# Kernel tuning notes

Measured on AMD Instinct MI355X. Metric: run time of the kernel, lower is better.

Reference implementation:

```python
import jax, jax.numpy as jnp
import numpy as np

B, S, D, H = 2, 2048, 1024, 16
DK = D // H


def setup_inputs() -> dict:
    key = jax.random.key(0)
    ks = jax.random.split(key, 12)
    sc = 0.02
    inp = {
        "q": jax.random.normal(ks[0], (B, S, D), jnp.float32),
        "k": jax.random.normal(ks[1], (B, S, D), jnp.float32),
        "v": jax.random.normal(ks[2], (B, S, D), jnp.float32),
        "mask": jnp.ones((B, S, S), jnp.int32),
        "Wq": jax.random.normal(ks[3], (D, D), jnp.float32) * sc,
        "bq": jnp.zeros((D,), jnp.float32),
        "Wk": jax.random.normal(ks[4], (D, D), jnp.float32) * sc,
        "bk": jnp.zeros((D,), jnp.float32),
        "Wv": jax.random.normal(ks[5], (D, D), jnp.float32) * sc,
        "bv": jnp.zeros((D,), jnp.float32),
        "Wo": jax.random.normal(ks[6], (D, D), jnp.float32) * sc,
        "bo": jnp.zeros((D,), jnp.float32),
    }
    return inp


def _split_heads(x):
    # [B,S,D] -> [B,H,S,DK]
    b, s, _ = x.shape
    return x.reshape(b, s, H, DK).transpose(0, 2, 1, 3)


def reference(q, k, v, mask, Wq, bq, Wk, bk, Wv, bv, Wo, bo):
    qh = _split_heads(q @ Wq.T + bq)
    kh = _split_heads(k @ Wk.T + bk)
    vh = _split_heads(v @ Wv.T + bv)
    scale = 1.0 / jnp.sqrt(jnp.float32(DK))
    scores = jnp.einsum("bhqd,bhkd->bhqk", qh, kh) * scale  # [B,H,S,S]
    scores = jnp.where(mask[:, None, :, :] == 0, jnp.float32(-1e9), scores)
    probs = jax.nn.softmax(scores, axis=-1)  # dropout p=0.0 -> identity
    out = jnp.einsum("bhqk,bhkd->bhqd", probs, vh)  # [B,H,S,DK]
    concat = out.transpose(0, 2, 1, 3).reshape(q.shape[0], -1, D)
    return concat @ Wo.T + bo
```

## Files before the change

### kernel.cpp

```cpp
#include <hip/hip_runtime.h>
#include <stdint.h>

#define Bsz 2
#define Ssz 2048
#define Dsz 1024
#define Hsz 16
#define DKsz 64

typedef __attribute__((ext_vector_type(8))) short sh8;
typedef __attribute__((ext_vector_type(4))) float fx4;
typedef __attribute__((ext_vector_type(16))) float fx16;
typedef __attribute__((ext_vector_type(4))) unsigned ux4;

__device__ __forceinline__ unsigned short f2bf(float x) {
  uint32_t u = __builtin_bit_cast(uint32_t, x);
  uint32_t r = (u + 0x7fffu + ((u >> 16) & 1u)) >> 16;
  return (unsigned short)r;
}

__device__ __forceinline__ fx4 mfma16(sh8 a, sh8 b, fx4 c) {
  return __builtin_amdgcn_mfma_f32_16x16x32_bf16(a, b, c, 0, 0, 0);
}

__device__ __forceinline__ fx16 mfma32(sh8 a, sh8 b, fx16 c) {
  return __builtin_amdgcn_mfma_f32_32x32x16_bf16(a, b, c, 0, 0, 0);
}

__device__ __forceinline__ void g2l16(const void* g, void* l) {
  __builtin_amdgcn_global_load_lds((const __attribute__((address_space(1))) void*)g,
                                   (__attribute__((address_space(3))) void*)l, 16, 0, 0);
}

__device__ __forceinline__ float fexp2(float x) {
#if __has_builtin(__builtin_amdgcn_exp2f)
  return __builtin_amdgcn_exp2f(x);
#else
  return exp2f(x);
#endif
}

__device__ __forceinline__ unsigned cvtpk(float lo, float hi) {
  unsigned r;
  asm("v_cvt_pk_bf16_f32 %0, %1, %2" : "=v"(r) : "v"(lo), "v"(hi));
  return r;
}

__device__ __forceinline__ void plswap(unsigned& a, unsigned& b) {
  asm("v_permlane32_swap_b32 %0, %1" : "+v"(a), "+v"(b));
}

__device__ __forceinline__ void build_pa(const fx16& p, sh8& pa0, sh8& pa1) {
  unsigned w0 = cvtpk(p[0], p[1]), w1 = cvtpk(p[2], p[3]);
  unsigned w2 = cvtpk(p[4], p[5]), w3 = cvtpk(p[6], p[7]);
  unsigned w4 = cvtpk(p[8], p[9]), w5 = cvtpk(p[10], p[11]);
  unsigned w6 = cvtpk(p[12], p[13]), w7 = cvtpk(p[14], p[15]);
  plswap(w0, w2);
  plswap(w1, w3);
  ux4 u0 = {w0, w1, w2, w3};
  pa0 = __builtin_bit_cast(sh8, u0);
  plswap(w4, w6);
  plswap(w5, w7);
  ux4 u1 = {w4, w5, w6, w7};
  pa1 = __builtin_bit_cast(sh8, u1);
}

__global__ __launch_bounds__(256) void convert_kernel(
    const float* __restrict__ wq, const float* __restrict__ wk, const float* __restrict__ wv,
    const float* __restrict__ wo, const int* __restrict__ mask,
    unsigned short* __restrict__ wqb, unsigned short* __restrict__ wkb,
    unsigned short* __restrict__ wvb, unsigned short* __restrict__ wob,
    int* __restrict__ flag) {
  const int NW = Dsz * Dsz / 4;
  const int NC = 4 * NW;
  const int NM = Bsz * Ssz * Ssz / 4;
  const int total = NC + NM;
  int bad = 0;
  for (int i = blockIdx.x * blockDim.x + threadIdx.x; i < total; i += gridDim.x * blockDim.x) {
    if (i >= NC) {
      int4 m = ((const int4*)mask)[i - NC];
      if (m.x == 0 || m.y == 0 || m.z == 0 || m.w == 0) bad = 1;
      continue;
    }
    int t = i / NW, off = i - t * NW;
    const float* src = (t == 0) ? wq : ((t == 1) ? wk : ((t == 2) ? wv : wo));
    unsigned short* dst = (t == 0) ? wqb : ((t == 1) ? wkb : ((t == 2) ? wvb : wob));
    float4 x = ((const float4*)src)[off];
    ushort4 o;
    o.x = f2bf(x.x); o.y = f2bf(x.y); o.z = f2bf(x.z); o.w = f2bf(x.w);
    ((ushort4*)dst)[off] = o;
  }
  if (bad) atomicAnd(flag, 0);
}

__global__ void flag_init_kernel(int* flag) {
  if (threadIdx.x == 0 && blockIdx.x == 0) flag[0] = 1;
}

__global__ __launch_bounds__(256) void proj_qkv_kernel(
    const float* __restrict__ qf, const float* __restrict__ kf, const float* __restrict__ vf,
    const unsigned short* __restrict__ wqb, const unsigned short* __restrict__ wkb,
    const unsigned short* __restrict__ wvb,
    const float* __restrict__ bq, const float* __restrict__ bk, const float* __restrict__ bv,
    unsigned short* __restrict__ qh, unsigned short* __restrict__ kh,
    unsigned short* __restrict__ vt) {
  __shared__ __align__(16) unsigned short SMEM[17408];
  unsigned short* As0 = SMEM;
  unsigned short* As1 = SMEM + 4096;
  unsigned short* Bs0 = SMEM + 8192;
  unsigned short* Bs1 = SMEM + 12288;
  unsigned short* Ts = SMEM;
  const int z = blockIdx.z;
  const float* X = (z == 0) ? qf : ((z == 1) ? kf : vf);
  const unsigned short* W = (z == 0) ? wqb : ((z == 1) ? wkb : wvb);
  const float* bias = (z == 0) ? bq : ((z == 1) ? bk : bv);
  const int m0 = blockIdx.x * 128, n0 = blockIdx.y * 128;
  const int tid = threadIdx.x, lane = tid & 63, wid = tid >> 6;
  const int wm = wid >> 1, wn = wid & 1;
  const int c = lane & 15, g = lane >> 4;
  fx4 acc[4][4] = {};

  auto LOADA = [&](int k0, float4* a) {
#pragma unroll
    for (int i = 0; i < 4; i++) {
      int c4 = i * 256 + tid;
      a[i] = *(const float4*)(X + (size_t)(m0 + (c4 >> 3)) * Dsz + k0 + (c4 & 7) * 4);
    }
  };
  auto WRITEA = [&](const float4* a, unsigned short* As) {
#pragma unroll
    for (int i = 0; i < 4; i++) {
      int c4 = i * 256 + tid;
      uint2 w;
      w.x = cvtpk(a[i].x, a[i].y);
      w.y = cvtpk(a[i].z, a[i].w);
      *(uint2*)&As[(c4 >> 3) * 32 + (c4 & 7) * 4] = w;
    }
  };
  auto G2LB = [&](int k0, unsigned short* Bs) {
#pragma unroll
    for (int i = 0; i < 2; i++) {
      int e = i * 256 + tid;
      g2l16(W + (size_t)(n0 + (e >> 2)) * Dsz + k0 + (e & 3) * 8,
            (char*)Bs + (size_t)(i * 256 + wid * 64) * 16);
    }
  };
  auto COMPUTE = [&](const unsigned short* As, const unsigned short* Bs) {
    sh8 af[4], bfr[4];
#pragma unroll
    for (int m = 0; m < 4; m++)
      af[m] = *(const sh8*)&As[(wm * 64 + m * 16 + c) * 32 + g * 8];
#pragma unroll
    for (int n = 0; n < 4; n++)
      bfr[n] = *(const sh8*)&Bs[(wn * 64 + n * 16 + c) * 32 + g * 8];
#pragma unroll
    for (int m = 0; m < 4; m++)
#pragma unroll
      for (int n = 0; n < 4; n++)
        acc[m][n] = mfma16(af[m], bfr[n], acc[m][n]);
  };

  float4 aA[4], aB[4];
  LOADA(0, aA);
  G2LB(0, Bs0);
  WRITEA(aA, As0);
  __syncthreads();
#pragma unroll 1
  for (int j = 0; j < 16; j++) {
    const int k0 = j * 64;
    if (k0 + 32 < Dsz) { LOADA(k0 + 32, aB); G2LB(k0 + 32, Bs1); }
    COMPUTE(As0, Bs0);
    if (k0 + 32 < Dsz) WRITEA(aB, As1);
    __syncthreads();
    if (k0 + 64 < Dsz) { LOADA(k0 + 64, aA); G2LB(k0 + 64, Bs0); }
    if (k0 + 32 < Dsz) COMPUTE(As1, Bs1);
    if (k0 + 64 < Dsz) WRITEA(aA, As0);
    __syncthreads();
  }

  const float CE = 0.18033688011112042f;
  if (z < 2) {
    unsigned short* O = (z == 0) ? qh : kh;
    const float sc = (z == 0) ? CE : 1.0f;
#pragma unroll
    for (int n = 0; n < 4; n++) {
      int j = n0 + wn * 64 + n * 16 + c;
      float bj = bias[j];
      int h = j >> 6, dk = j & 63;
#pragma unroll
      for (int m = 0; m < 4; m++)
#pragma unroll
        for (int r = 0; r < 4; r++) {
          int i = m0 + wm * 64 + m * 16 + g * 4 + r;
          int b = i >> 11, s = i & 2047;
          O[(((size_t)(b * Hsz + h) * Ssz + s) << 6) + dk] = f2bf((acc[m][n][r] + bj) * sc);
        }
    }
  } else {
#pragma unroll
    for (int n = 0; n < 4; n++) {
      int nl = wn * 64 + n * 16 + c;
      float bj = bias[n0 + nl];
#pragma unroll
      for (int m = 0; m < 4; m++)
#pragma unroll
        for (int r = 0; r < 4; r++) {
          int ml = wm * 64 + m * 16 + g * 4 + r;
          Ts[nl * 136 + ml] = f2bf(acc[m][n][r] + bj);
        }
    }
    __syncthreads();
    int b = m0 >> 11, sbase = m0 & 2047;
#pragma unroll
    for (int it = 0; it < 8; it++) {
      int ch = it * 256 + tid;
      int row = ch >> 4, off = ch & 15;
      sh8 dv = *(const sh8*)&Ts[row * 136 + off * 8];
      int j = n0 + row;
      int h = j >> 6, dk = j & 63;
      *(sh8*)&vt[(size_t)((b * Hsz + h) * DKsz + dk) * Ssz + sbase + off * 8] = dv;
    }
  }
}

__global__ __launch_bounds__(512, 4) void attn_kernel(
    const unsigned short* __restrict__ qh, const unsigned short* __restrict__ kh,
    const unsigned short* __restrict__ vt, const int* __restrict__ mask,
    const int* __restrict__ flag, unsigned short* __restrict__ concat) {
  __shared__ __align__(16) unsigned short SM[2][2][2][4096];
  const int tid = threadIdx.x, lane = tid & 63, wid = tid >> 6;
  const int grp = wid >> 2, w4 = wid & 3;
  const int fid = blockIdx.y * gridDim.x + blockIdx.x;
  const int logical = (fid & 7) * 64 + (fid >> 3);
  const int bh = logical >> 4, qblk = logical & 15;
  const int b = bh >> 4, h = bh & 15;
  const int q0 = qblk * 128 + w4 * 32;
  const int c = lane & 31, hi = lane >> 5;
  const int cs = c & 7;
  const int kvbase = grp * (Ssz / 2);
  const unsigned short* Qb = qh + ((size_t)bh * Ssz + q0) * DKsz;
  const unsigned short* Kb = kh + (size_t)bh * Ssz * DKsz;
  const unsigned short* Vb = vt + (size_t)bh * DKsz * Ssz;
  const int ch0 = w4 * 128 + lane;
  const int ch1 = ch0 + 64;
  const int r0 = ch0 >> 3, sl0 = (ch0 & 7) ^ (r0 & 7);
  const int r1 = ch1 >> 3, sl1 = (ch1 & 7) ^ (r1 & 7);
  const int koff0 = r0 * DKsz + sl0 * 8, koff1 = r1 * DKsz + sl1 * 8;
  const size_t voff0 = (size_t)r0 * Ssz + sl0 * 8, voff1 = (size_t)r1 * Ssz + sl1 * 8;

  sh8 qf[4];
#pragma unroll
  for (int ks = 0; ks < 4; ks++)
    qf[ks] = *(const sh8*)&Qb[(size_t)c * DKsz + ks * 16 + hi * 8];
  const bool allones = (flag[0] != 0);
  float lsum = 0.f;
  fx16 o0 = {}, o1 = {};

  auto STAGE = [&](int bufi, int kv0) {
    const unsigned short* ksrc = Kb + (size_t)kv0 * DKsz;
    char* kdst = (char*)&SM[0][grp][bufi][0] + w4 * 2048;
    g2l16(ksrc + koff0, kdst);
    g2l16(ksrc + koff1, kdst + 1024);
    const unsigned short* vsrc = Vb + kv0;
    char* vdst = (char*)&SM[1][grp][bufi][0] + w4 * 2048;
    g2l16(vsrc + voff0, vdst);
    g2l16(vsrc + voff1, vdst + 1024);
  };

  const int NT = (Ssz / 2) / 64;
  STAGE(0, kvbase);
  asm volatile("s_waitcnt vmcnt(0)" ::: "memory");
  __builtin_amdgcn_s_barrier();
  asm volatile("" ::: "memory");

  for (int t = 0; t < NT; ++t) {
    const int cur = t & 1;
    const int kv0 = kvbase + t * 64;
    if (t + 1 < NT) STAGE(cur ^ 1, kv0 + 64);
    const unsigned short* Kt = &SM[0][grp][cur][0];
    const unsigned short* Vt = &SM[1][grp][cur][0];
    fx16 s0 = {}, s1 = {};
    __builtin_amdgcn_s_setprio(1);
#pragma unroll
    for (int ks = 0; ks < 4; ks++) {
      int sl = (2 * ks + hi) ^ cs;
      sh8 ka = *(const sh8*)&Kt[(c * 8 + sl) * 8];
      sh8 kb2 = *(const sh8*)&Kt[((32 + c) * 8 + sl) * 8];
      s0 = mfma32(ka, qf[ks], s0);
      s1 = mfma32(kb2, qf[ks], s1);
    }
    __builtin_amdgcn_s_setprio(0);
    if (!allones) {
      const int* mrow = mask + ((size_t)b * Ssz + (q0 + c)) * Ssz + kv0;
#pragma unroll
      for (int r = 0; r < 16; r++) {
        int kv = (r & 3) + 8 * (r >> 2) + 4 * hi;
        if (mrow[kv] == 0) s0[r] = -1e9f;
        if (mrow[32 + kv] == 0) s1[r] = -1e9f;
      }
    }
    fx16 p0v, p1v;
#pragma unroll
    for (int r = 0; r < 16; r++) {
      p0v[r] = fexp2(s0[r]);
      p1v[r] = fexp2(s1[r]);
    }
    sh8 pa[4];
    build_pa(p0v, pa[0], pa[1]);
    build_pa(p1v, pa[2], pa[3]);
    __builtin_amdgcn_s_setprio(1);
#pragma unroll
    for (int ks = 0; ks < 4; ks++) {
      int sl = (2 * ks + hi) ^ cs;
      sh8 v0f = *(const sh8*)&Vt[(c * 8 + sl) * 8];
      sh8 v1f = *(const sh8*)&Vt[((32 + c) * 8 + sl) * 8];
      o0 = mfma32(v0f, pa[ks], o0);
      o1 = mfma32(v1f, pa[ks], o1);
    }
    __builtin_amdgcn_s_setprio(0);
    float sm[16];
#pragma unroll
    for (int r = 0; r < 16; r++) sm[r] = p0v[r] + p1v[r];
#pragma unroll
    for (int w = 8; w >= 1; w >>= 1)
#pragma unroll
      for (int r = 0; r < w; r++) sm[r] += sm[r + w];
    lsum += sm[0];
    asm volatile("s_waitcnt vmcnt(0)" ::: "memory");
    __builtin_amdgcn_s_barrier();
    asm volatile("" ::: "memory");
  }

  float* CB = (float*)&SM[0][0][0][0];
  float* CBl = CB + 4 * 32 * 68;
  if (grp == 1) {
#pragma unroll
    for (int k4 = 0; k4 < 4; k4++) {
      fx4 a = {o0[4 * k4], o0[4 * k4 + 1], o0[4 * k4 + 2], o0[4 * k4 + 3]};
      *(fx4*)&CB[(w4 * 32 + c) * 68 + 8 * k4 + 4 * hi] = a;
      fx4 bvv = {o1[4 * k4], o1[4 * k4 + 1], o1[4 * k4 + 2], o1[4 * k4 + 3]};
      *(fx4*)&CB[(w4 * 32 + c) * 68 + 32 + 8 * k4 + 4 * hi] = bvv;
    }
    CBl[w4 * 64 + hi * 32 + c] = lsum;
  }
  __syncthreads();
  if (grp == 0) {
#pragma unroll
    for (int k4 = 0; k4 < 4; k4++) {
      fx4 a = *(const fx4*)&CB[(w4 * 32 + c) * 68 + 8 * k4 + 4 * hi];
      o0[4 * k4] += a[0]; o0[4 * k4 + 1] += a[1]; o0[4 * k4 + 2] += a[2]; o0[4 * k4 + 3] += a[3];
      fx4 bvv = *(const fx4*)&CB[(w4 * 32 + c) * 68 + 32 + 8 * k4 + 4 * hi];
      o1[4 * k4] += bvv[0]; o1[4 * k4 + 1] += bvv[1]; o1[4 * k4 + 2] += bvv[2]; o1[4 * k4 + 3] += bvv[3];
    }
    lsum += CBl[w4 * 64 + hi * 32 + c];
    lsum += __shfl_xor(lsum, 32);
    float linv = 1.0f / lsum;
    unsigned short* Ob = concat + ((size_t)b * Ssz + q0 + c) * Dsz + h * DKsz;
#pragma unroll
    for (int rg = 0; rg < 4; rg++) {
      ushort4 w;
      w.x = f2bf(o0[rg * 4 + 0] * linv);
      w.y = f2bf(o0[rg * 4 + 1] * linv);
      w.z = f2bf(o0[rg * 4 + 2] * linv);
      w.w = f2bf(o0[rg * 4 + 3] * linv);
      *(ushort4*)&Ob[8 * rg + 4 * hi] = w;
      ushort4 w2;
      w2.x = f2bf(o1[rg * 4 + 0] * linv);
      w2.y = f2bf(o1[rg * 4 + 1] * linv);
      w2.z = f2bf(o1[rg * 4 + 2] * linv);
      w2.w = f2bf(o1[rg * 4 + 3] * linv);
      *(ushort4*)&Ob[32 + 8 * rg + 4 * hi] = w2;
    }
  }
}

__global__ __launch_bounds__(256) void outproj_kernel(
    const unsigned short* __restrict__ Xc, const unsigned short* __restrict__ wob,
    const float* __restrict__ bo, float* __restrict__ out) {
  __shared__ __align__(16) unsigned short As[128 * 32];
  __shared__ __align__(16) unsigned short Bs[128 * 32];
  const int m0 = blockIdx.x * 128, n0 = blockIdx.y * 128;
  const int tid = threadIdx.x, lane = tid & 63, wid = tid >> 6;
  const int wm = wid >> 1, wn = wid & 1;
  const int c = lane & 15, g = lane >> 4;
  fx4 acc[4][4] = {};
  for (int k0 = 0; k0 < Dsz; k0 += 32) {
#pragma unroll
    for (int i = 0; i < 2; i++) {
      int e = i * 256 + tid;
      g2l16(Xc + (size_t)(m0 + (e >> 2)) * Dsz + k0 + (e & 3) * 8,
            (char*)As + (size_t)(i * 256 + wid * 64) * 16);
      g2l16(wob + (size_t)(n0 + (e >> 2)) * Dsz + k0 + (e & 3) * 8,
            (char*)Bs + (size_t)(i * 256 + wid * 64) * 16);
    }
    __syncthreads();
    sh8 af[4], bfr[4];
#pragma unroll
    for (int m = 0; m < 4; m++)
      af[m] = *(const sh8*)&As[(wm * 64 + m * 16 + c) * 32 + g * 8];
#pragma unroll
    for (int n = 0; n < 4; n++)
      bfr[n] = *(const sh8*)&Bs[(wn * 64 + n * 16 + c) * 32 + g * 8];
#pragma unroll
    for (int m = 0; m < 4; m++)
#pragma unroll
      for (int n = 0; n < 4; n++)
        acc[m][n] = mfma16(af[m], bfr[n], acc[m][n]);
    __syncthreads();
  }
#pragma unroll
  for (int n = 0; n < 4; n++) {
    int j = n0 + wn * 64 + n * 16 + c;
    float bj = bo[j];
#pragma unroll
    for (int m = 0; m < 4; m++)
#pragma unroll
      for (int r = 0; r < 4; r++) {
        int i = m0 + wm * 64 + m * 16 + g * 4 + r;
        out[(size_t)i * Dsz + j] = acc[m][n][r] + bj;
      }
  }
}

extern "C" void kernel_launch(void* const* d_in, const int* in_sizes, int n_in,
                              void* d_out, int out_size, void* d_ws, size_t ws_size,
                              hipStream_t stream) {
  const float* q = (const float*)d_in[0];
  const float* k = (const float*)d_in[1];
  const float* v = (const float*)d_in[2];
  const int* mask = (const int*)d_in[3];
  const float* Wq = (const float*)d_in[4];
  const float* bq = (const float*)d_in[5];
  const float* Wk = (const float*)d_in[6];
  const float* bk = (const float*)d_in[7];
  const float* Wv = (const float*)d_in[8];
  const float* bv = (const float*)d_in[9];
  const float* Wo = (const float*)d_in[10];
  const float* bo = (const float*)d_in[11];
  float* out = (float*)d_out;
  char* ws = (char*)d_ws;
  const size_t MB = 1 << 20;
  unsigned short* wqb = (unsigned short*)(ws + 0 * MB);
  unsigned short* wkb = (unsigned short*)(ws + 2 * MB);
  unsigned short* wvb = (unsigned short*)(ws + 4 * MB);
  unsigned short* wob = (unsigned short*)(ws + 6 * MB);
  unsigned short* qhp = (unsigned short*)(ws + 8 * MB);
  unsigned short* khp = (unsigned short*)(ws + 16 * MB);
  unsigned short* vtp = (unsigned short*)(ws + 24 * MB);
  unsigned short* cc  = (unsigned short*)(ws + 32 * MB);
  int* flag = (int*)(ws + 40 * MB);

  hipLaunchKernelGGL(flag_init_kernel, dim3(1), dim3(64), 0, stream, flag);
  hipLaunchKernelGGL(convert_kernel, dim3(1024), dim3(256), 0, stream,
                     Wq, Wk, Wv, Wo, mask, wqb, wkb, wvb, wob, flag);
  hipLaunchKernelGGL(proj_qkv_kernel, dim3(32, 8, 3), dim3(256), 0, stream,
                     q, k, v, wqb, wkb, wvb, bq, bk, bv, qhp, khp, vtp);
  hipLaunchKernelGGL(attn_kernel, dim3(16, 32), dim3(512), 0, stream,
                     qhp, khp, vtp, mask, flag, cc);
  hipLaunchKernelGGL(outproj_kernel, dim3(32, 8), dim3(256), 0, stream,
                     cc, wob, bo, out);
}
```

Before: 139.1 us.

## Deepen QKV projection prefetch pipeline and stage Q/K epilogue stores through LDS

The QKV projection main loop becomes a single-step pipeline. A-operand register loads are issued two k-steps ahead, and partial vmcnt waits with raw s_barrier replace full __syncthreads, so global latency overlaps with MFMA work. The Q/K epilogue now writes bf16 results into shared memory first and then emits 16-byte vectorized global stores, replacing scattered 2-byte stores. This adds LDS traffic and an extra barrier, and it depends on the hand-counted vmcnt values being correct.

```diff
diff --git a/kernel.cpp b/kernel.cpp
--- a/kernel.cpp
+++ b/kernel.cpp
@@ -104,10 +104,6 @@
     unsigned short* __restrict__ qh, unsigned short* __restrict__ kh,
     unsigned short* __restrict__ vt) {
   __shared__ __align__(16) unsigned short SMEM[17408];
-  unsigned short* As0 = SMEM;
-  unsigned short* As1 = SMEM + 4096;
-  unsigned short* Bs0 = SMEM + 8192;
-  unsigned short* Bs1 = SMEM + 12288;
   unsigned short* Ts = SMEM;
   const int z = blockIdx.z;
   const float* X = (z == 0) ? qf : ((z == 1) ? kf : vf);
@@ -118,40 +114,49 @@
   const int wm = wid >> 1, wn = wid & 1;
   const int c = lane & 15, g = lane >> 4;
   fx4 acc[4][4] = {};
-
-  auto LOADA = [&](int k0, float4* a) {
+  const int NSTEP = Dsz / 32;
+
+  float4 rA[2][4];
+
+  auto LOADA = [&](int t, float4* r) {
+    const int k0 = t * 32;
 #pragma unroll
     for (int i = 0; i < 4; i++) {
       int c4 = i * 256 + tid;
-      a[i] = *(const float4*)(X + (size_t)(m0 + (c4 >> 3)) * Dsz + k0 + (c4 & 7) * 4);
+      r[i] = *(const float4*)(X + (size_t)(m0 + (c4 >> 3)) * Dsz + k0 + (c4 & 7) * 4);
     }
   };
-  auto WRITEA = [&](const float4* a, unsigned short* As) {
+  auto WRITEA = [&](const float4* r, int buf) {
+    unsigned short* dst = SMEM + buf * 4096;
 #pragma unroll
     for (int i = 0; i < 4; i++) {
       int c4 = i * 256 + tid;
       uint2 w;
-      w.x = cvtpk(a[i].x, a[i].y);
-      w.y = cvtpk(a[i].z, a[i].w);
-      *(uint2*)&As[(c4 >> 3) * 32 + (c4 & 7) * 4] = w;
+      w.x = cvtpk(r[i].x, r[i].y);
+      w.y = cvtpk(r[i].z, r[i].w);
+      *(uint2*)&dst[(c4 >> 3) * 32 + (c4 & 7) * 4] = w;
     }
   };
-  auto G2LB = [&](int k0, unsigned short* Bs) {
+  auto G2LB = [&](int t, int buf) {
+    const int k0 = t * 32;
+    unsigned short* dst = SMEM + 8192 + buf * 4096;
 #pragma unroll
     for (int i = 0; i < 2; i++) {
       int e = i * 256 + tid;
       g2l16(W + (size_t)(n0 + (e >> 2)) * Dsz + k0 + (e & 3) * 8,
-            (char*)Bs + (size_t)(i * 256 + wid * 64) * 16);
+            (char*)dst + (size_t)(i * 256 + wid * 64) * 16);
     }
   };
-  auto COMPUTE = [&](const unsigned short* As, const unsigned short* Bs) {
+  auto COMPUTE = [&](int buf) {
+    const unsigned short* A_ = SMEM + buf * 4096;
+    const unsigned short* B_ = SMEM + 8192 + buf * 4096;
     sh8 af[4], bfr[4];
 #pragma unroll
     for (int m = 0; m < 4; m++)
-      af[m] = *(const sh8*)&As[(wm * 64 + m * 16 + c) * 32 + g * 8];
+      af[m] = *(const sh8*)&A_[(wm * 64 + m * 16 + c) * 32 + g * 8];
 #pragma unroll
     for (int n = 0; n < 4; n++)
-      bfr[n] = *(const sh8*)&Bs[(wn * 64 + n * 16 + c) * 32 + g * 8];
+      bfr[n] = *(const sh8*)&B_[(wn * 64 + n * 16 + c) * 32 + g * 8];
 #pragma unroll
     for (int m = 0; m < 4; m++)
 #pragma unroll
@@ -159,23 +164,31 @@
         acc[m][n] = mfma16(af[m], bfr[n], acc[m][n]);
   };
 
-  float4 aA[4], aB[4];
-  LOADA(0, aA);
-  G2LB(0, Bs0);
-  WRITEA(aA, As0);
+  LOADA(0, rA[0]);
+  G2LB(0, 0);
+  LOADA(1, rA[1]);
+  WRITEA(rA[0], 0);
+  asm volatile("s_waitcnt vmcnt(4)" ::: "memory");
+  __builtin_amdgcn_s_barrier();
+  asm volatile("" ::: "memory");
+
+#pragma unroll 1
+  for (int t = 0; t < NSTEP; ++t) {
+    const int cur = t & 1;
+    if (t + 1 < NSTEP) G2LB(t + 1, cur ^ 1);
+    if (t + 2 < NSTEP) LOADA(t + 2, rA[t & 1]);
+    COMPUTE(cur);
+    if (t + 1 < NSTEP) {
+      WRITEA(rA[(t + 1) & 1], cur ^ 1);
+      if (t + 2 < NSTEP)
+        asm volatile("s_waitcnt vmcnt(4)" ::: "memory");
+      else
+        asm volatile("s_waitcnt vmcnt(0)" ::: "memory");
+      __builtin_amdgcn_s_barrier();
+      asm volatile("" ::: "memory");
+    }
+  }
   __syncthreads();
-#pragma unroll 1
-  for (int j = 0; j < 16; j++) {
-    const int k0 = j * 64;
-    if (k0 + 32 < Dsz) { LOADA(k0 + 32, aB); G2LB(k0 + 32, Bs1); }
-    COMPUTE(As0, Bs0);
-    if (k0 + 32 < Dsz) WRITEA(aB, As1);
-    __syncthreads();
-    if (k0 + 64 < Dsz) { LOADA(k0 + 64, aA); G2LB(k0 + 64, Bs0); }
-    if (k0 + 32 < Dsz) COMPUTE(As1, Bs1);
-    if (k0 + 64 < Dsz) WRITEA(aA, As0);
-    __syncthreads();
-  }
 
   const float CE = 0.18033688011112042f;
   if (z < 2) {
@@ -183,17 +196,27 @@
     const float sc = (z == 0) ? CE : 1.0f;
 #pragma unroll
     for (int n = 0; n < 4; n++) {
-      int j = n0 + wn * 64 + n * 16 + c;
-      float bj = bias[j];
+      int nl = wn * 64 + n * 16 + c;
+      float bj = bias[n0 + nl];
+#pragma unroll
+      for (int m = 0; m < 4; m++)
+#pragma unroll
+        for (int r = 0; r < 4; r++) {
+          int ml = wm * 64 + m * 16 + g * 4 + r;
+          Ts[ml * 136 + nl] = f2bf((acc[m][n][r] + bj) * sc);
+        }
+    }
+    __syncthreads();
+#pragma unroll
+    for (int it = 0; it < 8; it++) {
+      int ch = it * 256 + tid;
+      int row = ch >> 4, off = ch & 15;
+      sh8 dv = *(const sh8*)&Ts[row * 136 + off * 8];
+      int i = m0 + row;
+      int b = i >> 11, s = i & 2047;
+      int j = n0 + off * 8;
       int h = j >> 6, dk = j & 63;
-#pragma unroll
-      for (int m = 0; m < 4; m++)
-#pragma unroll
-        for (int r = 0; r < 4; r++) {
-          int i = m0 + wm * 64 + m * 16 + g * 4 + r;
-          int b = i >> 11, s = i & 2047;
-          O[(((size_t)(b * Hsz + h) * Ssz + s) << 6) + dk] = f2bf((acc[m][n][r] + bj) * sc);
-        }
+      *(sh8*)&O[(((size_t)(b * Hsz + h) * Ssz + s) << 6) + dk] = dv;
     }
   } else {
 #pragma unroll
```

Measured after the change: 215.9 us. 1.55x slower.

## Load fp32 A tiles directly to LDS with swizzle, stage Q/K epilogue stores

Applied to the files above, without the earlier changes.

The QKV projection now copies fp32 activation tiles straight into LDS through async global-to-LDS copies with an XOR swizzle, converting to bf16 only when fragments are read, instead of loading into registers and writing bf16 to LDS. The double-buffered software pipeline is replaced by a single-buffer loop with two barriers per k-step. The Q/K epilogue is restaged through LDS so it issues 16-byte coalesced stores instead of scattered 2-byte stores. Losing the double buffering removes load/compute overlap and doubles LDS traffic for A, which could offset the gains.

```diff
diff --git a/kernel.cpp b/kernel.cpp
--- a/kernel.cpp
+++ b/kernel.cpp
@@ -104,10 +104,8 @@
     unsigned short* __restrict__ qh, unsigned short* __restrict__ kh,
     unsigned short* __restrict__ vt) {
   __shared__ __align__(16) unsigned short SMEM[17408];
-  unsigned short* As0 = SMEM;
-  unsigned short* As1 = SMEM + 4096;
-  unsigned short* Bs0 = SMEM + 8192;
-  unsigned short* Bs1 = SMEM + 12288;
+  float* Afp = (float*)SMEM;
+  unsigned short* Bs = SMEM + 8192;
   unsigned short* Ts = SMEM;
   const int z = blockIdx.z;
   const float* X = (z == 0) ? qf : ((z == 1) ? kf : vf);
@@ -117,38 +115,34 @@
   const int tid = threadIdx.x, lane = tid & 63, wid = tid >> 6;
   const int wm = wid >> 1, wn = wid & 1;
   const int c = lane & 15, g = lane >> 4;
+  const int rsw = c & 7;
   fx4 acc[4][4] = {};
-
-  auto LOADA = [&](int k0, float4* a) {
+  for (int k0 = 0; k0 < Dsz; k0 += 32) {
 #pragma unroll
     for (int i = 0; i < 4; i++) {
-      int c4 = i * 256 + tid;
-      a[i] = *(const float4*)(X + (size_t)(m0 + (c4 >> 3)) * Dsz + k0 + (c4 & 7) * 4);
-    }
-  };
-  auto WRITEA = [&](const float4* a, unsigned short* As) {
-#pragma unroll
-    for (int i = 0; i < 4; i++) {
-      int c4 = i * 256 + tid;
-      uint2 w;
-      w.x = cvtpk(a[i].x, a[i].y);
-      w.y = cvtpk(a[i].z, a[i].w);
-      *(uint2*)&As[(c4 >> 3) * 32 + (c4 & 7) * 4] = w;
-    }
-  };
-  auto G2LB = [&](int k0, unsigned short* Bs) {
+      int ch = i * 256 + tid;
+      int row = ch >> 3, sl = (ch & 7) ^ (row & 7);
+      g2l16(X + (size_t)(m0 + row) * Dsz + k0 + sl * 4,
+            (char*)Afp + (size_t)(i * 256 + wid * 64) * 16);
+    }
 #pragma unroll
     for (int i = 0; i < 2; i++) {
       int e = i * 256 + tid;
       g2l16(W + (size_t)(n0 + (e >> 2)) * Dsz + k0 + (e & 3) * 8,
             (char*)Bs + (size_t)(i * 256 + wid * 64) * 16);
     }
-  };
-  auto COMPUTE = [&](const unsigned short* As, const unsigned short* Bs) {
+    __syncthreads();
     sh8 af[4], bfr[4];
 #pragma unroll
-    for (int m = 0; m < 4; m++)
-      af[m] = *(const sh8*)&As[(wm * 64 + m * 16 + c) * 32 + g * 8];
+    for (int m = 0; m < 4; m++) {
+      int row = wm * 64 + m * 16 + c;
+      fx4 lo = *(const fx4*)&Afp[row * 32 + ((2 * g) ^ rsw) * 4];
+      fx4 hi = *(const fx4*)&Afp[row * 32 + ((2 * g + 1) ^ rsw) * 4];
+      unsigned w0 = cvtpk(lo[0], lo[1]), w1 = cvtpk(lo[2], lo[3]);
+      unsigned w2 = cvtpk(hi[0], hi[1]), w3 = cvtpk(hi[2], hi[3]);
+      ux4 u = {w0, w1, w2, w3};
+      af[m] = __builtin_bit_cast(sh8, u);
+    }
 #pragma unroll
     for (int n = 0; n < 4; n++)
       bfr[n] = *(const sh8*)&Bs[(wn * 64 + n * 16 + c) * 32 + g * 8];
@@ -157,23 +151,6 @@
 #pragma unroll
       for (int n = 0; n < 4; n++)
         acc[m][n] = mfma16(af[m], bfr[n], acc[m][n]);
-  };
-
-  float4 aA[4], aB[4];
-  LOADA(0, aA);
-  G2LB(0, Bs0);
-  WRITEA(aA, As0);
-  __syncthreads();
-#pragma unroll 1
-  for (int j = 0; j < 16; j++) {
-    const int k0 = j * 64;
-    if (k0 + 32 < Dsz) { LOADA(k0 + 32, aB); G2LB(k0 + 32, Bs1); }
-    COMPUTE(As0, Bs0);
-    if (k0 + 32 < Dsz) WRITEA(aB, As1);
-    __syncthreads();
-    if (k0 + 64 < Dsz) { LOADA(k0 + 64, aA); G2LB(k0 + 64, Bs0); }
-    if (k0 + 32 < Dsz) COMPUTE(As1, Bs1);
-    if (k0 + 64 < Dsz) WRITEA(aA, As0);
     __syncthreads();
   }
 
@@ -183,17 +160,27 @@
     const float sc = (z == 0) ? CE : 1.0f;
 #pragma unroll
     for (int n = 0; n < 4; n++) {
-      int j = n0 + wn * 64 + n * 16 + c;
-      float bj = bias[j];
+      int nl = wn * 64 + n * 16 + c;
+      float bj = bias[n0 + nl];
+#pragma unroll
+      for (int m = 0; m < 4; m++)
+#pragma unroll
+        for (int r = 0; r < 4; r++) {
+          int ml = wm * 64 + m * 16 + g * 4 + r;
+          Ts[ml * 136 + nl] = f2bf((acc[m][n][r] + bj) * sc);
+        }
+    }
+    __syncthreads();
+#pragma unroll
+    for (int it = 0; it < 8; it++) {
+      int ch = it * 256 + tid;
+      int row = ch >> 4, off = ch & 15;
+      sh8 dv = *(const sh8*)&Ts[row * 136 + off * 8];
+      int i = m0 + row;
+      int b = i >> 11, s = i & 2047;
+      int j = n0 + off * 8;
       int h = j >> 6, dk = j & 63;
-#pragma unroll
-      for (int m = 0; m < 4; m++)
-#pragma unroll
-        for (int r = 0; r < 4; r++) {
-          int i = m0 + wm * 64 + m * 16 + g * 4 + r;
-          int b = i >> 11, s = i & 2047;
-          O[(((size_t)(b * Hsz + h) * Ssz + s) << 6) + dk] = f2bf((acc[m][n][r] + bj) * sc);
-        }
+      *(sh8*)&O[(((size_t)(b * Hsz + h) * Ssz + s) << 6) + dk] = dv;
     }
   } else {
 #pragma unroll
```

After: 151.6 us. 8.9% more time.
